# Performance work log

Hardware: AMD Instinct MI355X
Metric: run time of the kernel (lower is better)

The kernel has to match this reference:

```python
import jax, jax.numpy as jnp
import numpy as np

IMG_HEIGHT = 416.0
# standard YOLOv3 anchors, keyed by grid size
ANCHORS_13 = np.array([[116.0, 90.0], [156.0, 198.0], [373.0, 326.0]], dtype=np.float32)
ANCHORS_26 = np.array([[30.0, 61.0], [62.0, 45.0], [59.0, 119.0]], dtype=np.float32)
ANCHORS_52 = np.array([[10.0, 13.0], [16.0, 30.0], [33.0, 23.0]], dtype=np.float32)


def _decode(output, thresh, t, anchors):
    # output: [B, C, H, W] -> [B, H, W, 3, 5+nc]
    B, C, H, W = output.shape
    o = output.transpose(0, 2, 3, 1).reshape(B, H, W, 3, -1)
    conf = o[..., 0]                         # [B,H,W,3]
    mask = conf > thresh
    # grid indices (original: index[:,1]=row, index[:,2]=col, index[:,3]=anchor)
    rows = jnp.arange(H, dtype=o.dtype)[None, :, None, None]   # broadcast over B,W,3
    cols = jnp.arange(W, dtype=o.dtype)[None, None, :, None]
    n = jnp.broadcast_to(jnp.arange(B, dtype=o.dtype)[:, None, None, None], conf.shape)
    cy = (rows + o[..., 2]) * t
    cx = (cols + o[..., 1]) * t
    aw = anchors[:, 0]                        # [3]
    ah = anchors[:, 1]
    w = aw * jnp.exp(o[..., 3])
    h = ah * jnp.exp(o[..., 4])
    boxes = jnp.stack([n, cx, cy, w, h], axis=-1)             # [B,H,W,3,5]
    boxes = jnp.where(mask[..., None], boxes, jnp.zeros((), o.dtype))
    return boxes.reshape(-1, 5)


def setup_inputs() -> dict:
    key = jax.random.key(0)
    k1, k2, k3 = jax.random.split(key, 3)
    return {
        "output_13": jax.random.normal(k1, (32, 255, 13, 13), dtype=jnp.float32),
        "output_26": jax.random.normal(k2, (32, 255, 26, 26), dtype=jnp.float32),
        "output_52": jax.random.normal(k3, (32, 255, 52, 52), dtype=jnp.float32),
        "thresh": jnp.float32(0.5),
    }


def reference(output_13, output_26, output_52, thresh):
    a13 = jnp.asarray(ANCHORS_13)
    a26 = jnp.asarray(ANCHORS_26)
    a52 = jnp.asarray(ANCHORS_52)
    boxes_13 = _decode(output_13, thresh, IMG_HEIGHT / 13.0, a13)
    boxes_26 = _decode(output_26, thresh, IMG_HEIGHT / 26.0, a26)
    boxes_52 = _decode(output_52, thresh, IMG_HEIGHT / 52.0, a52)
    return jnp.concatenate([boxes_13, boxes_26, boxes_52], axis=0)
```

## Files before the change

kernel.cpp:

```cpp
#include <hip/hip_runtime.h>

constexpr int N13 = 32 * 13 * 13 * 3;
constexpr int N26 = 32 * 26 * 26 * 3;
constexpr int N52 = 32 * 52 * 52 * 3;
constexpr int NTOT = N13 + N26 + N52;

template <int H>
__device__ __forceinline__ void decode_head(const float* __restrict__ in,
                                            float* __restrict__ out,
                                            int r, float thresh,
                                            float aw0, float ah0,
                                            float aw1, float ah1,
                                            float aw2, float ah2) {
    constexpr int W = H;
    constexpr int PLANE = H * W;
    constexpr float t = 416.0f / (float)H;

    const int a    = r % 3;
    const int cell = r / 3;
    const int x    = cell % W;
    const int rest = cell / W;
    const int y    = rest % H;
    const int b    = rest / H;

    const float* base = in + ((((size_t)b * 255 + (size_t)a * 85) * H + y) * W + x);

    const float conf = base[0];
    const float o1   = base[PLANE * 1];
    const float o2   = base[PLANE * 2];
    const float o3   = base[PLANE * 3];
    const float o4   = base[PLANE * 4];

    const bool m = conf > thresh;

    const float aw = (a == 0) ? aw0 : ((a == 1) ? aw1 : aw2);
    const float ah = (a == 0) ? ah0 : ((a == 1) ? ah1 : ah2);

    const float n  = m ? (float)b : 0.0f;
    const float cx = m ? ((float)x + o1) * t : 0.0f;
    const float cy = m ? ((float)y + o2) * t : 0.0f;
    const float w  = m ? aw * __expf(o3) : 0.0f;
    const float h  = m ? ah * __expf(o4) : 0.0f;

    float* o = out + (size_t)r * 5;
    o[0] = n;
    o[1] = cx;
    o[2] = cy;
    o[3] = w;
    o[4] = h;
}

__global__ __launch_bounds__(256) void yolo_decode_all(
    const float* __restrict__ in13,
    const float* __restrict__ in26,
    const float* __restrict__ in52,
    const float* __restrict__ thp,
    float* __restrict__ out) {
    const int r = blockIdx.x * 256 + threadIdx.x;
    const float thresh = *thp;
    if (r < N13) {
        decode_head<13>(in13, out, r, thresh,
                        116.0f, 90.0f, 156.0f, 198.0f, 373.0f, 326.0f);
    } else if (r < N13 + N26) {
        decode_head<26>(in26, out + (size_t)N13 * 5, r - N13, thresh,
                        30.0f, 61.0f, 62.0f, 45.0f, 59.0f, 119.0f);
    } else if (r < NTOT) {
        decode_head<52>(in52, out + (size_t)(N13 + N26) * 5, r - (N13 + N26), thresh,
                        10.0f, 13.0f, 16.0f, 30.0f, 33.0f, 23.0f);
    }
}

extern "C" void kernel_launch(void* const* d_in, const int* in_sizes, int n_in,
                              void* d_out, int out_size, void* d_ws, size_t ws_size,
                              hipStream_t stream) {
    const float* in13 = (const float*)d_in[0];
    const float* in26 = (const float*)d_in[1];
    const float* in52 = (const float*)d_in[2];
    const float* thp  = (const float*)d_in[3];
    float* out = (float*)d_out;

    const int blocks = (NTOT + 255) / 256;
    yolo_decode_all<<<blocks, 256, 0, stream>>>(in13, in26, in52, thp, out);
}
```

Baseline: 130.6 us.

## Process one cell per thread and stage outputs in LDS for vectorized stores

Each thread now decodes all three anchors for one grid cell, so input reads are contiguous across threads along the spatial dimension. The 15 output floats per cell are staged in shared memory and then written out cooperatively as float4 stores. The goal is to replace the strided, poorly coalesced global loads and 20-byte-strided stores. In exchange there are fewer threads, a block-wide barrier, and an LDS footprint per block.

```diff
diff --git a/kernel.cpp b/kernel.cpp
--- a/kernel.cpp
+++ b/kernel.cpp
@@ -1,53 +1,68 @@
 #include <hip/hip_runtime.h>
 
-constexpr int N13 = 32 * 13 * 13 * 3;
-constexpr int N26 = 32 * 26 * 26 * 3;
-constexpr int N52 = 32 * 52 * 52 * 3;
-constexpr int NTOT = N13 + N26 + N52;
+constexpr int B_IMG = 32;
+constexpr int N13 = B_IMG * 13 * 13 * 3;
+constexpr int N26 = B_IMG * 26 * 26 * 3;
+
+constexpr int CELLS_PER_BLK = 256;
+constexpr int BLK13 = (B_IMG * 13 * 13 + CELLS_PER_BLK - 1) / CELLS_PER_BLK;
+constexpr int BLK26 = (B_IMG * 26 * 26 + CELLS_PER_BLK - 1) / CELLS_PER_BLK;
+constexpr int BLK52 = (B_IMG * 52 * 52 + CELLS_PER_BLK - 1) / CELLS_PER_BLK;
+constexpr int NBLK  = BLK13 + BLK26 + BLK52;
 
 template <int H>
-__device__ __forceinline__ void decode_head(const float* __restrict__ in,
-                                            float* __restrict__ out,
-                                            int r, float thresh,
-                                            float aw0, float ah0,
-                                            float aw1, float ah1,
-                                            float aw2, float ah2) {
+__device__ __forceinline__ void decode_head_blk(
+    const float* __restrict__ in,
+    float* __restrict__ outf,
+    int blk, int tid, float thresh,
+    float aw0, float ah0, float aw1, float ah1, float aw2, float ah2) {
     constexpr int W = H;
     constexpr int PLANE = H * W;
+    constexpr int NCELLS = B_IMG * PLANE;
     constexpr float t = 416.0f / (float)H;
 
-    const int a    = r % 3;
-    const int cell = r / 3;
-    const int x    = cell % W;
-    const int rest = cell / W;
-    const int y    = rest % H;
-    const int b    = rest / H;
+    __shared__ float lds[CELLS_PER_BLK * 15];
 
-    const float* base = in + ((((size_t)b * 255 + (size_t)a * 85) * H + y) * W + x);
+    const int cell0  = blk * CELLS_PER_BLK;
+    const int nvalid = min(CELLS_PER_BLK, NCELLS - cell0);
+    const int cell   = cell0 + tid;
 
-    const float conf = base[0];
-    const float o1   = base[PLANE * 1];
-    const float o2   = base[PLANE * 2];
-    const float o3   = base[PLANE * 3];
-    const float o4   = base[PLANE * 4];
+    if (tid < nvalid) {
+        const int img = cell / PLANE;
+        const int cip = cell - img * PLANE;
+        const int y   = cip / W;
+        const int x   = cip - y * W;
+        const float fx = (float)x, fy = (float)y, fb = (float)img;
 
-    const bool m = conf > thresh;
+#pragma unroll
+        for (int a = 0; a < 3; ++a) {
+            const float* base = in + (size_t)(img * 255 + a * 85) * PLANE + cip;
+            const float conf = base[0];
+            const float o1   = base[PLANE * 1];
+            const float o2   = base[PLANE * 2];
+            const float o3   = base[PLANE * 3];
+            const float o4   = base[PLANE * 4];
 
-    const float aw = (a == 0) ? aw0 : ((a == 1) ? aw1 : aw2);
-    const float ah = (a == 0) ? ah0 : ((a == 1) ? ah1 : ah2);
+            const bool m = conf > thresh;
+            const float aw = (a == 0) ? aw0 : ((a == 1) ? aw1 : aw2);
+            const float ah = (a == 0) ? ah0 : ((a == 1) ? ah1 : ah2);
 
-    const float n  = m ? (float)b : 0.0f;
-    const float cx = m ? ((float)x + o1) * t : 0.0f;
-    const float cy = m ? ((float)y + o2) * t : 0.0f;
-    const float w  = m ? aw * __expf(o3) : 0.0f;
-    const float h  = m ? ah * __expf(o4) : 0.0f;
+            float* s = &lds[(tid * 3 + a) * 5];
+            s[0] = m ? fb : 0.0f;
+            s[1] = m ? (fx + o1) * t : 0.0f;
+            s[2] = m ? (fy + o2) * t : 0.0f;
+            s[3] = m ? aw * __expf(o3) : 0.0f;
+            s[4] = m ? ah * __expf(o4) : 0.0f;
+        }
+    }
+    __syncthreads();
 
-    float* o = out + (size_t)r * 5;
-    o[0] = n;
-    o[1] = cx;
-    o[2] = cy;
-    o[3] = w;
-    o[4] = h;
+    const int nvec = (nvalid * 15) >> 2;
+    float4* ov = (float4*)(outf + (size_t)cell0 * 15);
+    const float4* sv = (const float4*)lds;
+    for (int i = tid; i < nvec; i += CELLS_PER_BLK) {
+        ov[i] = sv[i];
+    }
 }
 
 __global__ __launch_bounds__(256) void yolo_decode_all(
@@ -56,17 +71,18 @@
     const float* __restrict__ in52,
     const float* __restrict__ thp,
     float* __restrict__ out) {
-    const int r = blockIdx.x * 256 + threadIdx.x;
+    const int tid = threadIdx.x;
     const float thresh = *thp;
-    if (r < N13) {
-        decode_head<13>(in13, out, r, thresh,
-                        116.0f, 90.0f, 156.0f, 198.0f, 373.0f, 326.0f);
-    } else if (r < N13 + N26) {
-        decode_head<26>(in26, out + (size_t)N13 * 5, r - N13, thresh,
-                        30.0f, 61.0f, 62.0f, 45.0f, 59.0f, 119.0f);
-    } else if (r < NTOT) {
-        decode_head<52>(in52, out + (size_t)(N13 + N26) * 5, r - (N13 + N26), thresh,
-                        10.0f, 13.0f, 16.0f, 30.0f, 33.0f, 23.0f);
+    const int blk = blockIdx.x;
+    if (blk < BLK13) {
+        decode_head_blk<13>(in13, out, blk, tid, thresh,
+                            116.0f, 90.0f, 156.0f, 198.0f, 373.0f, 326.0f);
+    } else if (blk < BLK13 + BLK26) {
+        decode_head_blk<26>(in26, out + (size_t)N13 * 5, blk - BLK13, tid, thresh,
+                            30.0f, 61.0f, 62.0f, 45.0f, 59.0f, 119.0f);
+    } else {
+        decode_head_blk<52>(in52, out + (size_t)(N13 + N26) * 5, blk - (BLK13 + BLK26), tid, thresh,
+                            10.0f, 13.0f, 16.0f, 30.0f, 33.0f, 23.0f);
     }
 }
 
@@ -79,6 +95,5 @@
     const float* thp  = (const float*)d_in[3];
     float* out = (float*)d_out;
 
-    const int blocks = (NTOT + 255) / 256;
-    yolo_decode_all<<<blocks, 256, 0, stream>>>(in13, in26, in52, thp, out);
+    yolo_decode_all<<<NBLK, 256, 0, stream>>>(in13, in26, in52, thp, out);
 }
```

Result: no change. 130.0 us (-0.5%).
